# Kernel optimization log

Hardware: AMD Instinct MI355X
Metric: run time of the kernel (lower is better)

## Reference

```python
import jax, jax.numpy as jnp
import numpy as np
import math

NODE_DIM = 256
HIDDEN = 128
HEADS = 8
HEAD_DIM = HIDDEN // HEADS
SCALE = math.sqrt(HEAD_DIM)
EPS_DIST = 1e-6
EPS_NORM = 1e-6
LN_EPS = 1e-5


def setup_inputs() -> dict:
    key = jax.random.key(0)
    ks = jax.random.split(key, 16)
    B, N = 2, 768
    node_feats = jax.random.normal(ks[0], (B, N, NODE_DIM), dtype=jnp.float32)
    positions = jax.random.normal(ks[1], (B, N, 2), dtype=jnp.float32)
    mask = jax.random.randint(ks[2], (B, N), 0, 2).astype(bool)
    s = 0.05
    return {
        "node_feats": node_feats,
        "positions": positions,
        "mask": mask,
        "Wq": jax.random.normal(ks[3], (NODE_DIM, HIDDEN), dtype=jnp.float32) * s,
        "Wk": jax.random.normal(ks[4], (NODE_DIM, HIDDEN), dtype=jnp.float32) * s,
        "Wv": jax.random.normal(ks[5], (NODE_DIM, HIDDEN), dtype=jnp.float32) * s,
        "W1": jax.random.normal(ks[6], (3, HIDDEN), dtype=jnp.float32) * s,
        "b1": jnp.zeros((HIDDEN,), dtype=jnp.float32),
        "W2": jax.random.normal(ks[7], (HIDDEN, HIDDEN), dtype=jnp.float32) * s,
        "b2": jnp.zeros((HIDDEN,), dtype=jnp.float32),
        "Wo": jax.random.normal(ks[8], (HIDDEN, NODE_DIM), dtype=jnp.float32) * s,
        "bo": jnp.zeros((NODE_DIM,), dtype=jnp.float32),
        "gamma": jnp.ones((NODE_DIM,), dtype=jnp.float32),
        "beta": jnp.zeros((NODE_DIM,), dtype=jnp.float32),
    }


def reference(node_feats, positions, mask, Wq, Wk, Wv, W1, b1, W2, b2, Wo, bo, gamma, beta):
    B, N, _ = node_feats.shape
    # projections -> [B, H, N, hd]
    q = (node_feats @ Wq).reshape(B, N, HEADS, HEAD_DIM).transpose(0, 2, 1, 3)
    k = (node_feats @ Wk).reshape(B, N, HEADS, HEAD_DIM).transpose(0, 2, 1, 3)
    v = (node_feats @ Wv).reshape(B, N, HEADS, HEAD_DIM).transpose(0, 2, 1, 3)

    # pairwise geometry: deltas [B, N, N, 2]
    deltas = positions[:, :, None, :] - positions[:, None, :, :]
    sq = (deltas ** 2).sum(-1)
    distances = jnp.sqrt(sq + EPS_DIST)  # [B, N, N]
    # F.normalize: divide by norm clamped to eps
    norm = jnp.sqrt(sq)[..., None]
    direction = deltas / jnp.maximum(norm, EPS_NORM)
    edge_geom = jnp.concatenate([direction, distances[..., None]], axis=-1)  # [B,N,N,3]

    # edge MLP -> [B, N, N, HIDDEN] (exact GELU as torch default)
    h = jax.nn.gelu(edge_geom @ W1 + b1, approximate=False)
    edge_bias = (h @ W2 + b2).reshape(B, N, N, HEADS, HEAD_DIM)
    # mean over head_dim, permute to [B, H, N, N]
    bias = edge_bias.mean(-1).transpose(0, 3, 1, 2)

    scores = jnp.einsum('bhid,bhjd->bhij', q, k) / SCALE + bias

    key_mask = mask[:, None, None, :]  # [B,1,1,N]
    neg = jnp.finfo(scores.dtype).min
    scores = jnp.where(key_mask, scores, neg)
    valid_key_rows = jnp.any(key_mask, axis=-1, keepdims=True)  # [B,1,1,1]

    mx = scores.max(axis=-1, keepdims=True)
    mx = jnp.where(valid_key_rows, mx, 0.0)
    scores = jnp.where(valid_key_rows, scores - mx, 0.0)
    w = jax.nn.softmax(scores, axis=-1)
    w = jnp.where(valid_key_rows, w, 0.0)
    w = jnp.nan_to_num(w, nan=0.0, posinf=0.0, neginf=0.0)
    # query mask
    w = w * mask[:, None, :, None].astype(w.dtype)
    # dropout is identity at eval time

    agg = jnp.einsum('bhij,bhjd->bhid', w, v)  # [B,H,N,hd]
    agg = agg.transpose(0, 2, 1, 3).reshape(B, N, HIDDEN)
    agg = agg @ Wo + bo

    mf = mask[..., None].astype(node_feats.dtype)
    agg = agg * mf
    nf = node_feats * mf

    x = nf + agg
    mu = x.mean(-1, keepdims=True)
    var = ((x - mu) ** 2).mean(-1, keepdims=True)
    return (x - mu) / jnp.sqrt(var + LN_EPS) * gamma + beta
```

## Files before the change

### kernel.cpp

```cpp
#include <hip/hip_runtime.h>
#include <float.h>
#include <math.h>

#define NODE_DIM 256
#define HIDDEN   128
#define HEADS    8
#define HEAD_DIM 16
#define NB       768
#define BATCH    2
#define NNODES   (BATCH * NB)
#define SEP      776

typedef _Float16 f16;
typedef _Float16 h2 __attribute__((ext_vector_type(2)));
typedef __fp16 fp16x2 __attribute__((ext_vector_type(2)));
union F2H { float f; h2 h; unsigned u; };
union V4H { float4 f; h2 h[4]; };

__device__ __forceinline__ h2 pkrtz(float a, float b) {
  fp16x2 r = __builtin_amdgcn_cvt_pkrtz(a, b);
  return __builtin_bit_cast(h2, r);
}

__device__ __forceinline__ float gelu_poly(float u) {
  u = fminf(fmaxf(u, -2.5f), 2.5f);
  float t = u * u;
  float r = fmaf(t, -4.08639e-4f, 7.64400e-3f);
  r = fmaf(t, r, -6.40405e-2f);
  r = fmaf(t, r, 3.985355e-1f);
  return u * fmaf(u, r, 0.5f);
}

__device__ __forceinline__ void edge_bias_one(const float* __restrict__ P,
    float ux, float uy, float dd, f16* __restrict__ se, int k) {
  h2 acc[8] = {{0,0},{0,0},{0,0},{0,0},{0,0},{0,0},{0,0},{0,0}};
#pragma unroll 4
  for (int ip = 0; ip < 64; ++ip) {
    const float4* Pc = (const float4*)(P + ip * 16);
    float4 A = Pc[0], Bc = Pc[1];
    float g0 = gelu_poly(fmaf(ux, A.x, fmaf(uy, A.y, fmaf(dd, A.z, A.w))));
    float g1 = gelu_poly(fmaf(ux, Bc.x, fmaf(uy, Bc.y, fmaf(dd, Bc.z, Bc.w))));
    h2 gp = pkrtz(g0, g1);
    const h2* Wp = (const h2*)(Pc + 2);
#pragma unroll
    for (int h = 0; h < 8; ++h) acc[h] += gp * Wp[h];
  }
#pragma unroll
  for (int h = 0; h < 8; ++h) {
    f16* rr = se + h * SEP + k;
    *rr = (f16)(*rr + (f16)(acc[h].x + acc[h].y));
  }
}

__device__ __forceinline__ void edge_bias_two(const float* __restrict__ P,
    float ux0, float uy0, float d0, float ux1, float uy1, float d1,
    f16* __restrict__ se, int k0, int k1) {
  h2 acc0[8] = {{0,0},{0,0},{0,0},{0,0},{0,0},{0,0},{0,0},{0,0}};
  h2 acc1[8] = {{0,0},{0,0},{0,0},{0,0},{0,0},{0,0},{0,0},{0,0}};
#pragma unroll 2
  for (int ip = 0; ip < 64; ++ip) {
    const float4* Pc = (const float4*)(P + ip * 16);
    float4 A = Pc[0], Bc = Pc[1];
    float g00 = gelu_poly(fmaf(ux0, A.x, fmaf(uy0, A.y, fmaf(d0, A.z, A.w))));
    float g01 = gelu_poly(fmaf(ux0, Bc.x, fmaf(uy0, Bc.y, fmaf(d0, Bc.z, Bc.w))));
    float g10 = gelu_poly(fmaf(ux1, A.x, fmaf(uy1, A.y, fmaf(d1, A.z, A.w))));
    float g11 = gelu_poly(fmaf(ux1, Bc.x, fmaf(uy1, Bc.y, fmaf(d1, Bc.z, Bc.w))));
    h2 gp0 = pkrtz(g00, g01);
    h2 gp1 = pkrtz(g10, g11);
    const h2* Wp = (const h2*)(Pc + 2);
#pragma unroll
    for (int h = 0; h < 8; ++h) {
      acc0[h] += gp0 * Wp[h];
      acc1[h] += gp1 * Wp[h];
    }
  }
#pragma unroll
  for (int h = 0; h < 8; ++h) {
    f16* r0 = se + h * SEP + k0;
    *r0 = (f16)(*r0 + (f16)(acc0[h].x + acc0[h].y));
    f16* r1 = se + h * SEP + k1;
    *r1 = (f16)(*r1 + (f16)(acc1[h].x + acc1[h].y));
  }
}

__global__ __launch_bounds__(256) void prep_kernel(
    const float* __restrict__ nf, const float* __restrict__ pos,
    const int* __restrict__ mask,
    const float* __restrict__ Wq, const float* __restrict__ Wk,
    const float* __restrict__ Wv, const float* __restrict__ W1,
    const float* __restrict__ b1, const float* __restrict__ W2,
    const float* __restrict__ b2, const float* __restrict__ Wo,
    float* __restrict__ qc, f16* __restrict__ kTcH, f16* __restrict__ vcH,
    unsigned* __restrict__ WoP,
    float* __restrict__ P, float* __restrict__ b2m,
    float* __restrict__ pcx, float* __restrict__ pcy,
    int* __restrict__ vlist, int* __restrict__ mlist, int* __restrict__ cnt) {
  int blk = blockIdx.x, t = threadIdx.x;

  if (blk < NNODES / 4) {
    int n0 = blk * 4;
    int b = n0 / NB;
    int lo = n0 - b * NB;
    __shared__ int accv;
    if (t == 0) accv = 0;
    __syncthreads();
    for (int jb = 0; jb < lo; jb += 256) {
      int j = jb + t;
      int mv = (j < lo) && (mask[b * NB + j] != 0);
      unsigned long long ball = __ballot(mv);
      if ((t & 63) == 0) atomicAdd(&accv, __popcll(ball));
    }
    __syncthreads();
    int cb = accv;
    int m0 = mask[n0] != 0, m1 = mask[n0 + 1] != 0, m2 = mask[n0 + 2] != 0,
        m3 = mask[n0 + 3] != 0;
    int civ[4] = {cb, cb + m0, cb + m0 + m1, cb + m0 + m1 + m2};
    int mv4[4] = {m0, m1, m2, m3};

    const float* x0 = nf + (size_t)(n0 + 0) * NODE_DIM;
    const float* x1 = nf + (size_t)(n0 + 1) * NODE_DIM;
    const float* x2 = nf + (size_t)(n0 + 2) * NODE_DIM;
    const float* x3 = nf + (size_t)(n0 + 3) * NODE_DIM;
    for (int id = t; id < 3 * HIDDEN; id += 256) {
      int m = id >> 7, c = id & 127;
      const float* W = (m == 0) ? Wq : (m == 1) ? Wk : Wv;
      float a0 = 0.f, a1 = 0.f, a2 = 0.f, a3 = 0.f;
      float e0 = 0.f, e1 = 0.f, e2 = 0.f, e3 = 0.f;
#pragma unroll 8
      for (int kk = 0; kk < NODE_DIM; kk += 2) {
        float w0 = W[kk * HIDDEN + c];
        float w1 = W[(kk + 1) * HIDDEN + c];
        a0 = fmaf(x0[kk], w0, a0);  e0 = fmaf(x0[kk + 1], w1, e0);
        a1 = fmaf(x1[kk], w0, a1);  e1 = fmaf(x1[kk + 1], w1, e1);
        a2 = fmaf(x2[kk], w0, a2);  e2 = fmaf(x2[kk + 1], w1, e2);
        a3 = fmaf(x3[kk], w0, a3);  e3 = fmaf(x3[kk + 1], w1, e3);
      }
      float acc[4] = {a0 + e0, a1 + e1, a2 + e2, a3 + e3};
#pragma unroll
      for (int n = 0; n < 4; ++n) {
        if (mv4[n]) {
          int slot = b * NB + civ[n];
          if (m == 0)      qc[(size_t)slot * HIDDEN + c] = acc[n];
          else if (m == 1) kTcH[((size_t)b * HIDDEN + c) * NB + civ[n]] = (f16)acc[n];
          else             vcH[(size_t)slot * HIDDEN + c] = (f16)acc[n];
        }
      }
    }
  } else if (blk < NNODES / 4 + 2) {
    int b = blk - NNODES / 4;
    __shared__ int wcnt[4];
    __shared__ int base2[2];
    if (t < 2) base2[t] = 0;
    __syncthreads();
    int lane = t & 63, w = t >> 6;
    for (int iter = 0; iter < NB / 256; ++iter) {
      int j = iter * 256 + t;
      int mv = mask[b * NB + j] != 0;
      unsigned long long ball = __ballot(mv);
      if (lane == 0) wcnt[w] = __popcll(ball);
      __syncthreads();
      int pv = 0;
      for (int i = 0; i < w; ++i) pv += wcnt[i];
      int pin = (lane == 0) ? 0 : __popcll(ball & (~0ull >> (64 - lane)));
      if (mv) {
        int p = base2[0] + pv + pin;
        vlist[b * NB + p] = j;
        pcx[b * NB + p] = pos[(b * NB + j) * 2];
        pcy[b * NB + p] = pos[(b * NB + j) * 2 + 1];
      } else {
        int pm = base2[1] + (w * 64 - pv) + (lane - pin);
        mlist[b * NB + pm] = j;
      }
      __syncthreads();
      if (t == 0) {
        int tot = wcnt[0] + wcnt[1] + wcnt[2] + wcnt[3];
        base2[0] += tot;
        base2[1] += 256 - tot;
      }
      __syncthreads();
    }
    int nv = base2[0];
    if (t == 0) cnt[b] = nv;
    int nvp8 = (nv + 7) & ~7;
    if (t < HIDDEN)
      for (int col = nv; col < nvp8; ++col)
        kTcH[((size_t)b * HIDDEN + t) * NB + col] = (f16)0.0f;
  } else if (blk == NNODES / 4 + 2) {
    __shared__ float w2s[HIDDEN * HEADS];
    for (int idx = t; idx < HIDDEN * HEADS; idx += 256) {
      int c = idx >> 3, h = idx & 7;
      float s = 0.0f;
      for (int d = 0; d < HEAD_DIM; ++d) s += W2[c * HIDDEN + h * HEAD_DIM + d];
      w2s[idx] = s * (1.0f / 16.0f);
    }
    if (t < HEADS) {
      float s = 0.0f;
      for (int d = 0; d < HEAD_DIM; ++d) s += b2[t * HEAD_DIM + d];
      b2m[t] = s * (1.0f / 16.0f);
    }
    __syncthreads();
    if (t < 64) {
      int c0 = 2 * t, c1 = 2 * t + 1;
      float* Pb = P + t * 16;
      Pb[0] = W1[c0]; Pb[1] = W1[HIDDEN + c0];
      Pb[2] = W1[2 * HIDDEN + c0]; Pb[3] = b1[c0];
      Pb[4] = W1[c1]; Pb[5] = W1[HIDDEN + c1];
      Pb[6] = W1[2 * HIDDEN + c1]; Pb[7] = b1[c1];
      h2* ph = (h2*)(Pb + 8);
#pragma unroll
      for (int h = 0; h < 8; ++h)
        ph[h] = (h2){(f16)w2s[c0 * 8 + h], (f16)w2s[c1 * 8 + h]};
    }
  } else {
    for (int k2 = 0; k2 < 64; ++k2) {
      F2H w;
      w.h = (h2){(f16)Wo[(2 * k2) * NODE_DIM + t],
                 (f16)Wo[(2 * k2 + 1) * NODE_DIM + t]};
      WoP[k2 * 256 + t] = w.u;
    }
  }
}

__global__ __launch_bounds__(256) void attn_kernel(
    const float* __restrict__ pcx, const float* __restrict__ pcy,
    const int* __restrict__ cnt, const int* __restrict__ vlist,
    const int* __restrict__ mlist, const float* __restrict__ P,
    const float* __restrict__ b2m, const float* __restrict__ qc,
    const f16* __restrict__ kTcH, const f16* __restrict__ vcH,
    const unsigned* __restrict__ WoP,
    const float* __restrict__ nf, const float* __restrict__ bo,
    const float* __restrict__ gamma, const float* __restrict__ beta,
    float* __restrict__ out) {
  int b = blockIdx.x & 1, ci = blockIdx.x >> 1;
  int t = threadIdx.x;
  int nv = cnt[b];
  if (ci >= nv) {
    int node = b * NB + mlist[b * NB + (ci - nv)];
    out[(size_t)node * NODE_DIM + t] = beta[t];
    return;
  }
  int node = b * NB + vlist[b * NB + ci];
  int slot = b * NB + ci;

  __shared__ __align__(16) unsigned char smem[21760];
  f16*   sE    = (f16*)smem;
  float* qs    = (float*)(smem + 12416);
  float* partD = (float*)(smem + 12928);
  float* aggL  = (float*)(smem + 21120);
  float* red   = (float*)(smem + 21632);
  float* invs  = (float*)(smem + 21664);

  if (t < HIDDEN) qs[t] = qc[(size_t)slot * HIDDEN + t];
  float pix = pcx[slot], piy = pcy[slot];
  __syncthreads();

  {
    int h = t >> 5, l = t & 31;
    const f16* kb = kTcH + ((size_t)b * HIDDEN + h * 16) * NB;
    h2 qp[16];
#pragma unroll
    for (int r = 0; r < 16; ++r) {
      f16 qh = (f16)qs[h * 16 + r];
      qp[r] = (h2){qh, qh};
    }
    h2 sc4 = {(f16)0.25f, (f16)0.25f};
    f16 bhh = (f16)b2m[h];
    h2 bh2 = {bhh, bhh};
    int n8 = (nv + 7) >> 3;
    for (int j8 = l; j8 < n8; j8 += 32) {
      h2 acc[4] = {{0, 0}, {0, 0}, {0, 0}, {0, 0}};
#pragma unroll
      for (int r = 0; r < 16; ++r) {
        V4H kv;
        kv.f = *(const float4*)(kb + (size_t)r * NB + j8 * 8);
        acc[0] += qp[r] * kv.h[0];
        acc[1] += qp[r] * kv.h[1];
        acc[2] += qp[r] * kv.h[2];
        acc[3] += qp[r] * kv.h[3];
      }
      V4H res;
#pragma unroll
      for (int p = 0; p < 4; ++p) res.h[p] = acc[p] * sc4 + bh2;
      *(float4*)(sE + h * SEP + j8 * 8) = res.f;
    }
  }
  __syncthreads();

  {
    int k0 = t, k1 = t + 256, k2 = t + 512;
    if (k0 < nv) {
      int s0 = b * NB + k0;
      float dx = pix - pcx[s0], dy = piy - pcy[s0];
      float sq = fmaf(dx, dx, dy * dy);
      float d0 = __builtin_amdgcn_sqrtf(sq + 1e-6f);
      float inv = fminf(__builtin_amdgcn_rsqf(sq), 1e6f);
      float ux0 = dx * inv, uy0 = dy * inv;
      if (k1 < nv) {
        int s1 = b * NB + k1;
        float dx1 = pix - pcx[s1], dy1 = piy - pcy[s1];
        float sq1 = fmaf(dx1, dx1, dy1 * dy1);
        float dd1 = __builtin_amdgcn_sqrtf(sq1 + 1e-6f);
        float inv1 = fminf(__builtin_amdgcn_rsqf(sq1), 1e6f);
        edge_bias_two(P, ux0, uy0, d0, dx1 * inv1, dy1 * inv1, dd1, sE, k0, k1);
      } else {
        edge_bias_one(P, ux0, uy0, d0, sE, k0);
      }
    }
    if (k2 < nv) {
      int s2 = b * NB + k2;
      float dx = pix - pcx[s2], dy = piy - pcy[s2];
      float sq = fmaf(dx, dx, dy * dy);
      float dd = __builtin_amdgcn_sqrtf(sq + 1e-6f);
      float inv = fminf(__builtin_amdgcn_rsqf(sq), 1e6f);
      edge_bias_one(P, dx * inv, dy * inv, dd, sE, k2);
    }
  }
  __syncthreads();

  {
    int h = t >> 5, l = t & 31;
    f16* row = sE + h * SEP;
    float m = -FLT_MAX;
    for (int jj = l; jj < nv; jj += 32) m = fmaxf(m, (float)row[jj]);
    for (int off = 16; off; off >>= 1) m = fmaxf(m, __shfl_down(m, off, 32));
    m = __shfl(m, 0, 32);
    float s = 0.0f;
    for (int jj = l; jj < nv; jj += 32) {
      float e = __expf((float)row[jj] - m);
      row[jj] = (f16)e;
      s += e;
    }
    for (int off = 16; off; off >>= 1) s += __shfl_down(s, off, 32);
    if (l == 0) invs[h] = 1.0f / s;
  }
  __syncthreads();

  {
    int o8 = t & 15, g = t >> 4;
    int h = o8 >> 1;
    h2 acc[4] = {{0, 0}, {0, 0}, {0, 0}, {0, 0}};
    for (int jj = g; jj < nv; jj += 16) {
      V4H vv;
      vv.f = *(const float4*)(vcH + (size_t)(b * NB + jj) * HIDDEN + o8 * 8);
      f16 w = sE[h * SEP + jj];
      h2 ww = {w, w};
      acc[0] += ww * vv.h[0];
      acc[1] += ww * vv.h[1];
      acc[2] += ww * vv.h[2];
      acc[3] += ww * vv.h[3];
    }
    float* pd = partD + g * HIDDEN + o8 * 8;
    pd[0] = (float)acc[0].x; pd[1] = (float)acc[0].y;
    pd[2] = (float)acc[1].x; pd[3] = (float)acc[1].y;
    pd[4] = (float)acc[2].x; pd[5] = (float)acc[2].y;
    pd[6] = (float)acc[3].x; pd[7] = (float)acc[3].y;
  }
  __syncthreads();
  if (t < HIDDEN) {
    float s = 0.0f;
#pragma unroll
    for (int g = 0; g < 16; ++g) s += partD[g * HIDDEN + t];
    aggL[t] = s * invs[t >> 4];
  }
  __syncthreads();

  {
    float y0 = bo[t], y1 = 0.f;
    const unsigned* wp = WoP + t;
    const float2* a2 = (const float2*)aggL;
#pragma unroll 4
    for (int k2 = 0; k2 < 64; ++k2) {
      F2H w;
      w.u = wp[(size_t)k2 * 256];
      float2 a = a2[k2];
      y0 = fmaf(a.x, (float)w.h.x, y0);
      y1 = fmaf(a.y, (float)w.h.y, y1);
    }
    float y = y0 + y1;
    float xv = nf[(size_t)node * NODE_DIM + t] + y;
    float s = xv, s2 = xv * xv;
    for (int off = 32; off; off >>= 1) {
      s += __shfl_down(s, off, 64);
      s2 += __shfl_down(s2, off, 64);
    }
    if ((t & 63) == 0) { red[t >> 6] = s; red[4 + (t >> 6)] = s2; }
    __syncthreads();
    s  = red[0] + red[1] + red[2] + red[3];
    s2 = red[4] + red[5] + red[6] + red[7];
    float mu = s * (1.0f / NODE_DIM);
    float var = fmaxf(s2 * (1.0f / NODE_DIM) - mu * mu, 0.0f);
    out[(size_t)node * NODE_DIM + t] =
        (xv - mu) * rsqrtf(var + 1e-5f) * gamma[t] + beta[t];
  }
}

extern "C" void kernel_launch(void* const* d_in, const int* in_sizes, int n_in,
                              void* d_out, int out_size, void* d_ws, size_t ws_size,
                              hipStream_t stream) {
  const float* nf    = (const float*)d_in[0];
  const float* pos   = (const float*)d_in[1];
  const int*   mask  = (const int*)  d_in[2];
  const float* Wq    = (const float*)d_in[3];
  const float* Wk    = (const float*)d_in[4];
  const float* Wv    = (const float*)d_in[5];
  const float* W1    = (const float*)d_in[6];
  const float* b1    = (const float*)d_in[7];
  const float* W2    = (const float*)d_in[8];
  const float* b2    = (const float*)d_in[9];
  const float* Wo    = (const float*)d_in[10];
  const float* bo    = (const float*)d_in[11];
  const float* gamma = (const float*)d_in[12];
  const float* beta  = (const float*)d_in[13];

  const int QKV = NNODES * HIDDEN;

  float*    ws   = (float*)d_ws;
  float*    qc   = ws;
  f16*      kTcH = (f16*)(qc + QKV);
  f16*      vcH  = kTcH + QKV;
  unsigned* WoP  = (unsigned*)(vcH + QKV);
  float*    P    = (float*)(WoP + 64 * 256);
  float*    b2m  = P + HIDDEN * 8;
  float*    pcx  = b2m + 8;
  float*    pcy  = pcx + NNODES;
  int*      vlist= (int*)(pcy + NNODES);
  int*      mlist= vlist + NNODES;
  int*      cnt  = mlist + NNODES;

  prep_kernel<<<NNODES / 4 + 4, 256, 0, stream>>>(
      nf, pos, mask, Wq, Wk, Wv, W1, b1, W2, b2, Wo,
      qc, kTcH, vcH, WoP, P, b2m, pcx, pcy, vlist, mlist, cnt);
  attn_kernel<<<NNODES, 256, 0, stream>>>(
      pcx, pcy, cnt, vlist, mlist, P, b2m, qc, kTcH, vcH, WoP,
      nf, bo, gamma, beta, (float*)d_out);
}
```

Baseline: 132.7 us.

## Split attention keys across two blocks with flash-style partial softmax merge

Splits each query's key range into two halves processed by separate blocks. Each block writes its partial weighted-V sum, max and sum to a workspace record, and a new merge kernel combines them with log-sum-exp rescaling before the Wo projection and LayerNorm. The goal is to double the grid size and cut per-block edge-MLP work from up to three keys per thread to two, which improves load balance and occupancy. In exchange it adds an extra kernel launch and a global round-trip for the partial results.

```diff
diff --git a/kernel.cpp b/kernel.cpp
--- a/kernel.cpp
+++ b/kernel.cpp
@@ -9,7 +9,8 @@
 #define NB       768
 #define BATCH    2
 #define NNODES   (BATCH * NB)
-#define SEP      776
+#define SEPP     392
+#define REC      144
 
 typedef _Float16 f16;
 typedef _Float16 h2 __attribute__((ext_vector_type(2)));
@@ -47,7 +48,7 @@
   }
 #pragma unroll
   for (int h = 0; h < 8; ++h) {
-    f16* rr = se + h * SEP + k;
+    f16* rr = se + h * SEPP + k;
     *rr = (f16)(*rr + (f16)(acc[h].x + acc[h].y));
   }
 }
@@ -76,9 +77,9 @@
   }
 #pragma unroll
   for (int h = 0; h < 8; ++h) {
-    f16* r0 = se + h * SEP + k0;
+    f16* r0 = se + h * SEPP + k0;
     *r0 = (f16)(*r0 + (f16)(acc0[h].x + acc0[h].y));
-    f16* r1 = se + h * SEP + k1;
+    f16* r1 = se + h * SEPP + k1;
     *r1 = (f16)(*r1 + (f16)(acc1[h].x + acc1[h].y));
   }
 }
@@ -221,16 +222,153 @@
   }
 }
 
-__global__ __launch_bounds__(256) void attn_kernel(
+__global__ __launch_bounds__(256) void attn_part_kernel(
     const float* __restrict__ pcx, const float* __restrict__ pcy,
-    const int* __restrict__ cnt, const int* __restrict__ vlist,
-    const int* __restrict__ mlist, const float* __restrict__ P,
+    const int* __restrict__ cnt, const float* __restrict__ P,
     const float* __restrict__ b2m, const float* __restrict__ qc,
     const f16* __restrict__ kTcH, const f16* __restrict__ vcH,
-    const unsigned* __restrict__ WoP,
-    const float* __restrict__ nf, const float* __restrict__ bo,
-    const float* __restrict__ gamma, const float* __restrict__ beta,
-    float* __restrict__ out) {
+    float* __restrict__ part) {
+  int half = blockIdx.x & 1, idx = blockIdx.x >> 1;
+  int b = idx & 1, ci = idx >> 1;
+  int t = threadIdx.x;
+  int nv = cnt[b];
+  if (ci >= nv) return;
+  int slot = b * NB + ci;
+  int H8 = (((nv + 1) >> 1) + 7) & ~7;
+  int klo = half * H8;
+  int khi = min(nv, klo + H8);
+  int kn = khi - klo;
+  float* rec = part + ((size_t)slot * 2 + half) * REC;
+  if (kn <= 0) {
+    if (t < 128) rec[t] = 0.f;
+    else if (t < 136) rec[t] = -3.0e38f;
+    else if (t < 144) rec[t] = 0.f;
+    return;
+  }
+
+  __shared__ __align__(16) unsigned char smem[15104];
+  f16*   sE    = (f16*)smem;
+  float* qs    = (float*)(smem + 6272);
+  float* partD = (float*)(smem + 6784);
+  float* ms    = (float*)(smem + 14976);
+  float* ss    = (float*)(smem + 15008);
+
+  if (t < HIDDEN) qs[t] = qc[(size_t)slot * HIDDEN + t];
+  float pix = pcx[slot], piy = pcy[slot];
+  __syncthreads();
+
+  {
+    int h = t >> 5, l = t & 31;
+    const f16* kb = kTcH + ((size_t)b * HIDDEN + h * 16) * NB + klo;
+    h2 qp[16];
+#pragma unroll
+    for (int r = 0; r < 16; ++r) {
+      f16 qh = (f16)qs[h * 16 + r];
+      qp[r] = (h2){qh, qh};
+    }
+    h2 sc4 = {(f16)0.25f, (f16)0.25f};
+    f16 bhh = (f16)b2m[h];
+    h2 bh2 = {bhh, bhh};
+    int n8 = (kn + 7) >> 3;
+    for (int j8 = l; j8 < n8; j8 += 32) {
+      h2 acc[4] = {{0, 0}, {0, 0}, {0, 0}, {0, 0}};
+#pragma unroll
+      for (int r = 0; r < 16; ++r) {
+        V4H kv;
+        kv.f = *(const float4*)(kb + (size_t)r * NB + j8 * 8);
+        acc[0] += qp[r] * kv.h[0];
+        acc[1] += qp[r] * kv.h[1];
+        acc[2] += qp[r] * kv.h[2];
+        acc[3] += qp[r] * kv.h[3];
+      }
+      V4H res;
+#pragma unroll
+      for (int p = 0; p < 4; ++p) res.h[p] = acc[p] * sc4 + bh2;
+      *(float4*)(sE + h * SEPP + j8 * 8) = res.f;
+    }
+  }
+  __syncthreads();
+
+  {
+    int k0 = t, k1 = t + 256;
+    if (k0 < kn) {
+      int s0 = b * NB + klo + k0;
+      float dx = pix - pcx[s0], dy = piy - pcy[s0];
+      float sq = fmaf(dx, dx, dy * dy);
+      float d0 = __builtin_amdgcn_sqrtf(sq + 1e-6f);
+      float inv = fminf(__builtin_amdgcn_rsqf(sq), 1e6f);
+      float ux0 = dx * inv, uy0 = dy * inv;
+      if (k1 < kn) {
+        int s1 = b * NB + klo + k1;
+        float dx1 = pix - pcx[s1], dy1 = piy - pcy[s1];
+        float sq1 = fmaf(dx1, dx1, dy1 * dy1);
+        float dd1 = __builtin_amdgcn_sqrtf(sq1 + 1e-6f);
+        float inv1 = fminf(__builtin_amdgcn_rsqf(sq1), 1e6f);
+        edge_bias_two(P, ux0, uy0, d0, dx1 * inv1, dy1 * inv1, dd1, sE, k0, k1);
+      } else {
+        edge_bias_one(P, ux0, uy0, d0, sE, k0);
+      }
+    }
+  }
+  __syncthreads();
+
+  {
+    int h = t >> 5, l = t & 31;
+    f16* row = sE + h * SEPP;
+    float m = -FLT_MAX;
+    for (int jj = l; jj < kn; jj += 32) m = fmaxf(m, (float)row[jj]);
+    for (int off = 16; off; off >>= 1) m = fmaxf(m, __shfl_down(m, off, 32));
+    m = __shfl(m, 0, 32);
+    float s = 0.0f;
+    for (int jj = l; jj < kn; jj += 32) {
+      float e = __expf((float)row[jj] - m);
+      row[jj] = (f16)e;
+      s += e;
+    }
+    for (int off = 16; off; off >>= 1) s += __shfl_down(s, off, 32);
+    if (l == 0) { ms[h] = m; ss[h] = s; }
+  }
+  __syncthreads();
+
+  {
+    int o8 = t & 15, g = t >> 4;
+    int h = o8 >> 1;
+    h2 acc[4] = {{0, 0}, {0, 0}, {0, 0}, {0, 0}};
+    for (int jj = g; jj < kn; jj += 16) {
+      V4H vv;
+      vv.f = *(const float4*)(vcH + (size_t)(b * NB + klo + jj) * HIDDEN + o8 * 8);
+      f16 w = sE[h * SEPP + jj];
+      h2 ww = {w, w};
+      acc[0] += ww * vv.h[0];
+      acc[1] += ww * vv.h[1];
+      acc[2] += ww * vv.h[2];
+      acc[3] += ww * vv.h[3];
+    }
+    float* pd = partD + g * HIDDEN + o8 * 8;
+    pd[0] = (float)acc[0].x; pd[1] = (float)acc[0].y;
+    pd[2] = (float)acc[1].x; pd[3] = (float)acc[1].y;
+    pd[4] = (float)acc[2].x; pd[5] = (float)acc[2].y;
+    pd[6] = (float)acc[3].x; pd[7] = (float)acc[3].y;
+  }
+  __syncthreads();
+  if (t < 128) {
+    float s = 0.0f;
+#pragma unroll
+    for (int g = 0; g < 16; ++g) s += partD[g * HIDDEN + t];
+    rec[t] = s;
+  } else if (t < 136) {
+    rec[t] = ms[t - 128];
+  } else if (t < 144) {
+    rec[t] = ss[t - 136];
+  }
+}
+
+__global__ __launch_bounds__(256) void attn_merge_kernel(
+    const int* __restrict__ cnt, const int* __restrict__ vlist,
+    const int* __restrict__ mlist, const float* __restrict__ part,
+    const unsigned* __restrict__ WoP, const float* __restrict__ nf,
+    const float* __restrict__ bo, const float* __restrict__ gamma,
+    const float* __restrict__ beta, float* __restrict__ out) {
   int b = blockIdx.x & 1, ci = blockIdx.x >> 1;
   int t = threadIdx.x;
   int nv = cnt[b];
@@ -242,125 +380,18 @@
   int node = b * NB + vlist[b * NB + ci];
   int slot = b * NB + ci;
 
-  __shared__ __align__(16) unsigned char smem[21760];
-  f16*   sE    = (f16*)smem;
-  float* qs    = (float*)(smem + 12416);
-  float* partD = (float*)(smem + 12928);
-  float* aggL  = (float*)(smem + 21120);
-  float* red   = (float*)(smem + 21632);
-  float* invs  = (float*)(smem + 21664);
-
-  if (t < HIDDEN) qs[t] = qc[(size_t)slot * HIDDEN + t];
-  float pix = pcx[slot], piy = pcy[slot];
-  __syncthreads();
-
-  {
-    int h = t >> 5, l = t & 31;
-    const f16* kb = kTcH + ((size_t)b * HIDDEN + h * 16) * NB;
-    h2 qp[16];
-#pragma unroll
-    for (int r = 0; r < 16; ++r) {
-      f16 qh = (f16)qs[h * 16 + r];
-      qp[r] = (h2){qh, qh};
-    }
-    h2 sc4 = {(f16)0.25f, (f16)0.25f};
-    f16 bhh = (f16)b2m[h];
-    h2 bh2 = {bhh, bhh};
-    int n8 = (nv + 7) >> 3;
-    for (int j8 = l; j8 < n8; j8 += 32) {
-      h2 acc[4] = {{0, 0}, {0, 0}, {0, 0}, {0, 0}};
-#pragma unroll
-      for (int r = 0; r < 16; ++r) {
-        V4H kv;
-        kv.f = *(const float4*)(kb + (size_t)r * NB + j8 * 8);
-        acc[0] += qp[r] * kv.h[0];
-        acc[1] += qp[r] * kv.h[1];
-        acc[2] += qp[r] * kv.h[2];
-        acc[3] += qp[r] * kv.h[3];
-      }
-      V4H res;
-#pragma unroll
-      for (int p = 0; p < 4; ++p) res.h[p] = acc[p] * sc4 + bh2;
-      *(float4*)(sE + h * SEP + j8 * 8) = res.f;
-    }
-  }
-  __syncthreads();
-
-  {
-    int k0 = t, k1 = t + 256, k2 = t + 512;
-    if (k0 < nv) {
-      int s0 = b * NB + k0;
-      float dx = pix - pcx[s0], dy = piy - pcy[s0];
-      float sq = fmaf(dx, dx, dy * dy);
-      float d0 = __builtin_amdgcn_sqrtf(sq + 1e-6f);
-      float inv = fminf(__builtin_amdgcn_rsqf(sq), 1e6f);
-      float ux0 = dx * inv, uy0 = dy * inv;
-      if (k1 < nv) {
-        int s1 = b * NB + k1;
-        float dx1 = pix - pcx[s1], dy1 = piy - pcy[s1];
-        float sq1 = fmaf(dx1, dx1, dy1 * dy1);
-        float dd1 = __builtin_amdgcn_sqrtf(sq1 + 1e-6f);
-        float inv1 = fminf(__builtin_amdgcn_rsqf(sq1), 1e6f);
-        edge_bias_two(P, ux0, uy0, d0, dx1 * inv1, dy1 * inv1, dd1, sE, k0, k1);
-      } else {
-        edge_bias_one(P, ux0, uy0, d0, sE, k0);
-      }
-    }
-    if (k2 < nv) {
-      int s2 = b * NB + k2;
-      float dx = pix - pcx[s2], dy = piy - pcy[s2];
-      float sq = fmaf(dx, dx, dy * dy);
-      float dd = __builtin_amdgcn_sqrtf(sq + 1e-6f);
-      float inv = fminf(__builtin_amdgcn_rsqf(sq), 1e6f);
-      edge_bias_one(P, dx * inv, dy * inv, dd, sE, k2);
-    }
-  }
-  __syncthreads();
-
-  {
-    int h = t >> 5, l = t & 31;
-    f16* row = sE + h * SEP;
-    float m = -FLT_MAX;
-    for (int jj = l; jj < nv; jj += 32) m = fmaxf(m, (float)row[jj]);
-    for (int off = 16; off; off >>= 1) m = fmaxf(m, __shfl_down(m, off, 32));
-    m = __shfl(m, 0, 32);
-    float s = 0.0f;
-    for (int jj = l; jj < nv; jj += 32) {
-      float e = __expf((float)row[jj] - m);
-      row[jj] = (f16)e;
-      s += e;
-    }
-    for (int off = 16; off; off >>= 1) s += __shfl_down(s, off, 32);
-    if (l == 0) invs[h] = 1.0f / s;
-  }
-  __syncthreads();
-
-  {
-    int o8 = t & 15, g = t >> 4;
-    int h = o8 >> 1;
-    h2 acc[4] = {{0, 0}, {0, 0}, {0, 0}, {0, 0}};
-    for (int jj = g; jj < nv; jj += 16) {
-      V4H vv;
-      vv.f = *(const float4*)(vcH + (size_t)(b * NB + jj) * HIDDEN + o8 * 8);
-      f16 w = sE[h * SEP + jj];
-      h2 ww = {w, w};
-      acc[0] += ww * vv.h[0];
-      acc[1] += ww * vv.h[1];
-      acc[2] += ww * vv.h[2];
-      acc[3] += ww * vv.h[3];
-    }
-    float* pd = partD + g * HIDDEN + o8 * 8;
-    pd[0] = (float)acc[0].x; pd[1] = (float)acc[0].y;
-    pd[2] = (float)acc[1].x; pd[3] = (float)acc[1].y;
-    pd[4] = (float)acc[2].x; pd[5] = (float)acc[2].y;
-    pd[6] = (float)acc[3].x; pd[7] = (float)acc[3].y;
-  }
-  __syncthreads();
+  __shared__ float aggL[HIDDEN];
+  __shared__ float red[8];
+
+  const float* r0 = part + (size_t)slot * 2 * REC;
+  const float* r1 = r0 + REC;
   if (t < HIDDEN) {
-    float s = 0.0f;
-#pragma unroll
-    for (int g = 0; g < 16; ++g) s += partD[g * HIDDEN + t];
-    aggL[t] = s * invs[t >> 4];
+    int h = t >> 4;
+    float m0 = r0[128 + h], m1 = r1[128 + h];
+    float M = fmaxf(m0, m1);
+    float e0 = __expf(m0 - M), e1 = __expf(m1 - M);
+    float l = fmaf(e0, r0[136 + h], e1 * r1[136 + h]);
+    aggL[t] = fmaf(e0, r0[t], e1 * r1[t]) / l;
   }
   __syncthreads();
 
@@ -426,11 +457,13 @@
   int*      vlist= (int*)(pcy + NNODES);
   int*      mlist= vlist + NNODES;
   int*      cnt  = mlist + NNODES;
+  float*    part = (float*)(cnt + 16);
 
   prep_kernel<<<NNODES / 4 + 4, 256, 0, stream>>>(
       nf, pos, mask, Wq, Wk, Wv, W1, b1, W2, b2, Wo,
       qc, kTcH, vcH, WoP, P, b2m, pcx, pcy, vlist, mlist, cnt);
-  attn_kernel<<<NNODES, 256, 0, stream>>>(
-      pcx, pcy, cnt, vlist, mlist, P, b2m, qc, kTcH, vcH, WoP,
-      nf, bo, gamma, beta, (float*)d_out);
-}
+  attn_part_kernel<<<2 * NNODES, 256, 0, stream>>>(
+      pcx, pcy, cnt, P, b2m, qc, kTcH, vcH, part);
+  attn_merge_kernel<<<NNODES, 256, 0, stream>>>(
+      cnt, vlist, mlist, part, WoP, nf, bo, gamma, beta, (float*)d_out);
+}
```

New measurement: 130.5 us. About the same (-1.7%).
